# Optimization experiments

Measured on AMD Instinct MI355X. Metric: run time of the kernel, lower is better.

## Reference

```python
import jax, jax.numpy as jnp
import numpy as np

BATCH = 4096
FEAT = 1024
HID = 1024


def setup_inputs() -> dict:
    key = jax.random.key(0)
    ks = jax.random.split(key, 11)
    s_x = 1.0 / np.sqrt(FEAT)
    s_h = 1.0 / np.sqrt(HID)
    return {
        "x": jax.random.normal(ks[0], (BATCH, FEAT), jnp.float32),
        "h_prev": jax.random.normal(ks[1], (BATCH, HID), jnp.float32),
        "c_prev": jax.random.normal(ks[2], (BATCH, HID), jnp.float32),
        # Dense(3*hidden) on x and h (keras Dense: y = x @ W + b)
        "W_ifo_x": jax.random.normal(ks[3], (FEAT, 3 * HID), jnp.float32) * s_x,
        "b_ifo_x": jnp.zeros((3 * HID,), jnp.float32),
        "W_ifo_h": jax.random.normal(ks[4], (HID, 3 * HID), jnp.float32) * s_h,
        "b_ifo_h": jnp.zeros((3 * HID,), jnp.float32),
        # Dense(hidden) on x and h for candidate 'a'
        "W_b_x": jax.random.normal(ks[5], (FEAT, HID), jnp.float32) * s_x,
        "b_b_x": jnp.zeros((HID,), jnp.float32),
        "W_b_h": jax.random.normal(ks[6], (HID, HID), jnp.float32) * s_h,
        "b_b_h": jnp.zeros((HID,), jnp.float32),
    }


def reference(x, h_prev, c_prev, W_ifo_x, b_ifo_x, W_ifo_h, b_ifo_h,
              W_b_x, b_b_x, W_b_h, b_b_h):
    # Fused gate projections: [B, 3H]
    ifo = jax.nn.sigmoid(x @ W_ifo_x + b_ifo_x + h_prev @ W_ifo_h + b_ifo_h)
    i, f, o = jnp.split(ifo, 3, axis=-1)
    a = jnp.tanh(x @ W_b_x + b_b_x + h_prev @ W_b_h + b_b_h)
    c = i * a + f * c_prev
    h = o * jnp.tanh(c)
    return (h, c)
```

## Files before the change

kernel.cpp:

```cpp
#include <hip/hip_runtime.h>
#include <hip/hip_bf16.h>
#include <stdint.h>
#include <stddef.h>


#define BATCH 4096
#define FEAT  1024
#define HID   1024
#define NCAT  4096
#define KCAT  2048

typedef __attribute__((ext_vector_type(8))) __bf16 bf16x8;
typedef __attribute__((ext_vector_type(4))) float  floatx4;

__device__ __forceinline__ unsigned short f2bf(float f) {
    __hip_bfloat16 b = __float2bfloat16(f);
    return *reinterpret_cast<unsigned short*>(&b);
}
__device__ __forceinline__ void gl2lds16(const unsigned short* g, unsigned short* l) {
    __builtin_amdgcn_global_load_lds(
        (const __attribute__((address_space(1))) void*)g,
        (__attribute__((address_space(3))) void*)l, 16, 0, 0);
}

#define TP_PAD 72
__global__ __launch_bounds__(256)
void pack_all(const float* __restrict__ x, const float* __restrict__ h,
              const float* __restrict__ Wix, const float* __restrict__ Wih,
              const float* __restrict__ Wbx, const float* __restrict__ Wbh,
              unsigned short* __restrict__ Xcat, unsigned short* __restrict__ Wt) {
    __shared__ unsigned short tile[64 * TP_PAD];
    const int t = threadIdx.x;
    const int b = blockIdx.x;
    if (b < BATCH) {
        const int m = b;
        const float* src = (t < 128) ? (x + (size_t)m * FEAT + t * 8)
                                     : (h + (size_t)m * HID + (t - 128) * 8);
        float4 v0 = *(const float4*)src;
        float4 v1 = *(const float4*)(src + 4);
        union { unsigned short s16[8]; uint4 v; } pk;
        pk.s16[0] = f2bf(v0.x); pk.s16[1] = f2bf(v0.y);
        pk.s16[2] = f2bf(v0.z); pk.s16[3] = f2bf(v0.w);
        pk.s16[4] = f2bf(v1.x); pk.s16[5] = f2bf(v1.y);
        pk.s16[6] = f2bf(v1.z); pk.s16[7] = f2bf(v1.w);
        *(uint4*)(Xcat + (size_t)m * KCAT + t * 8) = pk.v;
        return;
    }
    const int tid = b - BATCH;
    const int k0  = (tid & 31) * 64;
    const int q0  = (tid >> 5) * 64;
    const float* src; int stride, cb;
    if (q0 < 3072) { src = (k0 < FEAT) ? Wix : Wih; stride = 3072; cb = q0; }
    else           { src = (k0 < FEAT) ? Wbx : Wbh; stride = 1024; cb = q0 - 3072; }
    const int krow = (k0 < FEAT) ? k0 : (k0 - FEAT);
    {
        int kl = t >> 2;
        int c0 = (t & 3) * 16;
        const float* s = src + (size_t)(krow + kl) * stride + cb + c0;
        union { unsigned short s16[16]; uint4 v[2]; } tmp;
#pragma unroll
        for (int u = 0; u < 16; u += 4) {
            float4 v = *(const float4*)(s + u);
            tmp.s16[u + 0] = f2bf(v.x); tmp.s16[u + 1] = f2bf(v.y);
            tmp.s16[u + 2] = f2bf(v.z); tmp.s16[u + 3] = f2bf(v.w);
        }
        *(uint4*)&tile[kl * TP_PAD + c0]     = tmp.v[0];
        *(uint4*)&tile[kl * TP_PAD + c0 + 8] = tmp.v[1];
    }
    __syncthreads();
    {
        int nl = t >> 2, seg = t & 3;
        int q = q0 + nl;
        int g, j;
        if (q < 3072) { g = q >> 10; j = q & 1023; }
        else          { g = 3;       j = q - 3072; }
        int np = ((j >> 4) << 6) + (g << 4) + (j & 15);
        union { unsigned short s16[16]; uint4 v[2]; } pk;
#pragma unroll
        for (int u = 0; u < 16; ++u)
            pk.s16[u] = tile[(seg * 16 + u) * TP_PAD + nl];
        uint4* dst = (uint4*)(Wt + (size_t)np * KCAT + k0 + seg * 16);
        dst[0] = pk.v[0];
        dst[1] = pk.v[1];
    }
}

#define BM 128
#define BN 128
#define BK 32

__global__ __launch_bounds__(256)
void lstm_fused(const unsigned short* __restrict__ Xcat,
                const unsigned short* __restrict__ Wt,
                const float* __restrict__ c_prev,
                const float* __restrict__ bix, const float* __restrict__ bih,
                const float* __restrict__ bbx, const float* __restrict__ bbh,
                float* __restrict__ out_h, float* __restrict__ out_c) {
    __shared__ unsigned short As[BM * BK];
    __shared__ unsigned short Bs[BN * BK];
    const int t    = threadIdx.x;
    const int lane = t & 63;
    const int wave = t >> 6;
    const int wm   = (wave >> 1) * 64;
    const int wn   = (wave & 1) * 64;
    const int m0   = blockIdx.y * BM;
    const int n0   = blockIdx.x * BN;

    floatx4 acc[4][4];
#pragma unroll
    for (int i = 0; i < 4; ++i)
#pragma unroll
        for (int g = 0; g < 4; ++g) acc[i][g] = (floatx4){0.f, 0.f, 0.f, 0.f};

    const int lrow = t >> 2;
    const int cg   = ((t & 3) ^ (lrow + (lrow >> 2))) & 3;
    const int lcol = cg * 8;

    const int lm  = lane & 15;
    const int fcs = ((lane >> 4) ^ (lm + (lm >> 2))) & 3;

    for (int kk = 0; kk < KCAT; kk += BK) {
        __syncthreads();
        gl2lds16(Xcat + (size_t)(m0 + lrow)      * KCAT + kk + lcol, &As[t * 8]);
        gl2lds16(Xcat + (size_t)(m0 + lrow + 64) * KCAT + kk + lcol, &As[t * 8 + 2048]);
        gl2lds16(Wt   + (size_t)(n0 + lrow)      * KCAT + kk + lcol, &Bs[t * 8]);
        gl2lds16(Wt   + (size_t)(n0 + lrow + 64) * KCAT + kk + lcol, &Bs[t * 8 + 2048]);
        __syncthreads();

        bf16x8 a[4], b[4];
#pragma unroll
        for (int i = 0; i < 4; ++i)
            a[i] = *(const bf16x8*)&As[(wm + i * 16 + lm) * BK + fcs * 8];
#pragma unroll
        for (int g = 0; g < 4; ++g)
            b[g] = *(const bf16x8*)&Bs[(wn + g * 16 + lm) * BK + fcs * 8];
#pragma unroll
        for (int i = 0; i < 4; ++i)
#pragma unroll
            for (int g = 0; g < 4; ++g)
                acc[i][g] = __builtin_amdgcn_mfma_f32_16x16x32_bf16(a[i], b[g], acc[i][g], 0, 0, 0);
    }

    const int j  = (((n0 + wn) >> 6) << 4) + lm;
    const float bi = bix[j]           + bih[j];
    const float bf = bix[HID + j]     + bih[HID + j];
    const float bo = bix[2 * HID + j] + bih[2 * HID + j];
    const float ba = bbx[j]           + bbh[j];
#pragma unroll
    for (int i = 0; i < 4; ++i) {
#pragma unroll
        for (int r = 0; r < 4; ++r) {
            int m = m0 + wm + i * 16 + ((lane >> 4) * 4) + r;
            float pi = acc[i][0][r] + bi;
            float pf = acc[i][1][r] + bf;
            float po = acc[i][2][r] + bo;
            float pa = acc[i][3][r] + ba;
            float ig = 1.f / (1.f + __expf(-pi));
            float fg = 1.f / (1.f + __expf(-pf));
            float og = 1.f / (1.f + __expf(-po));
            float av = 2.f / (1.f + __expf(-2.f * pa)) - 1.f;
            float cp = c_prev[(size_t)m * HID + j];
            float cv = ig * av + fg * cp;
            float hv = og * (2.f / (1.f + __expf(-2.f * cv)) - 1.f);
            out_h[(size_t)m * HID + j] = hv;
            out_c[(size_t)m * HID + j] = cv;
        }
    }
}

__global__ void naive_lstm(const float* __restrict__ x, const float* __restrict__ h,
                           const float* __restrict__ cvp,
                           const float* __restrict__ Wix, const float* __restrict__ bix,
                           const float* __restrict__ Wih, const float* __restrict__ bih,
                           const float* __restrict__ Wbx, const float* __restrict__ bbx,
                           const float* __restrict__ Wbh, const float* __restrict__ bbh,
                           float* __restrict__ out_h, float* __restrict__ out_c) {
    const int j = blockIdx.x * 256 + threadIdx.x;
    const int m = blockIdx.y;
    float ai = 0.f, af = 0.f, ao = 0.f, aa = 0.f;
    for (int k = 0; k < FEAT; ++k) {
        float xk = x[(size_t)m * FEAT + k];
        ai += xk * Wix[(size_t)k * 3072 + j];
        af += xk * Wix[(size_t)k * 3072 + HID + j];
        ao += xk * Wix[(size_t)k * 3072 + 2 * HID + j];
        aa += xk * Wbx[(size_t)k * HID + j];
    }
    for (int k = 0; k < HID; ++k) {
        float hk = h[(size_t)m * HID + k];
        ai += hk * Wih[(size_t)k * 3072 + j];
        af += hk * Wih[(size_t)k * 3072 + HID + j];
        ao += hk * Wih[(size_t)k * 3072 + 2 * HID + j];
        aa += hk * Wbh[(size_t)k * HID + j];
    }
    ai += bix[j] + bih[j];
    af += bix[HID + j] + bih[HID + j];
    ao += bix[2 * HID + j] + bih[2 * HID + j];
    aa += bbx[j] + bbh[j];
    float ig = 1.f / (1.f + __expf(-ai));
    float fg = 1.f / (1.f + __expf(-af));
    float og = 1.f / (1.f + __expf(-ao));
    float av = 2.f / (1.f + __expf(-2.f * aa)) - 1.f;
    float cp = cvp[(size_t)m * HID + j];
    float cc = ig * av + fg * cp;
    float hh = og * (2.f / (1.f + __expf(-2.f * cc)) - 1.f);
    out_h[(size_t)m * HID + j] = hh;
    out_c[(size_t)m * HID + j] = cc;
}

extern "C" void kernel_launch(void* const* d_in, const int* in_sizes, int n_in,
                              void* d_out, int out_size, void* d_ws, size_t ws_size,
                              hipStream_t stream) {
    const float* x   = (const float*)d_in[0];
    const float* h   = (const float*)d_in[1];
    const float* c   = (const float*)d_in[2];
    const float* Wix = (const float*)d_in[3];
    const float* bix = (const float*)d_in[4];
    const float* Wih = (const float*)d_in[5];
    const float* bih = (const float*)d_in[6];
    const float* Wbx = (const float*)d_in[7];
    const float* bbx = (const float*)d_in[8];
    const float* Wbh = (const float*)d_in[9];
    const float* bbh = (const float*)d_in[10];

    float* out_h = (float*)d_out;
    float* out_c = out_h + (size_t)BATCH * HID;

    const size_t WT_BYTES = (size_t)NCAT * KCAT * 2;
    const size_t XC_BYTES = (size_t)BATCH * KCAT * 2;
    if (ws_size >= WT_BYTES + XC_BYTES) {
        unsigned short* Wt   = (unsigned short*)d_ws;
        unsigned short* Xcat = (unsigned short*)((char*)d_ws + WT_BYTES);
        pack_all<<<BATCH + 2048, 256, 0, stream>>>(x, h, Wix, Wih, Wbx, Wbh, Xcat, Wt);
        lstm_fused<<<dim3(NCAT / BN, BATCH / BM), 256, 0, stream>>>(
            Xcat, Wt, c, bix, bih, bbx, bbh, out_h, out_c);
    } else {
        naive_lstm<<<dim3(HID / 256, BATCH), 256, 0, stream>>>(
            x, h, c, Wix, bix, Wih, bih, Wbx, bbx, Wbh, bbh, out_h, out_c);
    }
}
```

Before: 228.8 us.

## Fuse activation bf16 conversion into GEMM A-tile loads, drop Xcat packing

Removes the separate pass that converts x and h_prev to a concatenated bf16 buffer. The GEMM kernel now loads fp32 activations directly from global memory, converts them to bf16 in registers, and stores them to LDS, while the weights still use the async global-to-LDS path. This saves a full write and re-read of the activation buffer, but every N-tile block re-reads the fp32 activations (twice the bytes of bf16) and runs the conversion redundantly. The synchronous register loads also add latency inside the main loop, and the LDS swizzle patterns change.

Measured after the change: 292.5 us. 1.28x slower.

```diff
diff --git a/kernel.cpp b/kernel.cpp
--- a/kernel.cpp
+++ b/kernel.cpp
@@ -25,30 +25,13 @@
 
 #define TP_PAD 72
 __global__ __launch_bounds__(256)
-void pack_all(const float* __restrict__ x, const float* __restrict__ h,
-              const float* __restrict__ Wix, const float* __restrict__ Wih,
-              const float* __restrict__ Wbx, const float* __restrict__ Wbh,
-              unsigned short* __restrict__ Xcat, unsigned short* __restrict__ Wt) {
+void wt_pack(const float* __restrict__ Wix, const float* __restrict__ Wih,
+             const float* __restrict__ Wbx, const float* __restrict__ Wbh,
+             unsigned short* __restrict__ Wt) {
     __shared__ unsigned short tile[64 * TP_PAD];
-    const int t = threadIdx.x;
-    const int b = blockIdx.x;
-    if (b < BATCH) {
-        const int m = b;
-        const float* src = (t < 128) ? (x + (size_t)m * FEAT + t * 8)
-                                     : (h + (size_t)m * HID + (t - 128) * 8);
-        float4 v0 = *(const float4*)src;
-        float4 v1 = *(const float4*)(src + 4);
-        union { unsigned short s16[8]; uint4 v; } pk;
-        pk.s16[0] = f2bf(v0.x); pk.s16[1] = f2bf(v0.y);
-        pk.s16[2] = f2bf(v0.z); pk.s16[3] = f2bf(v0.w);
-        pk.s16[4] = f2bf(v1.x); pk.s16[5] = f2bf(v1.y);
-        pk.s16[6] = f2bf(v1.z); pk.s16[7] = f2bf(v1.w);
-        *(uint4*)(Xcat + (size_t)m * KCAT + t * 8) = pk.v;
-        return;
-    }
-    const int tid = b - BATCH;
-    const int k0  = (tid & 31) * 64;
-    const int q0  = (tid >> 5) * 64;
+    const int t  = threadIdx.x;
+    const int k0 = (blockIdx.x & 31) * 64;
+    const int q0 = (blockIdx.x >> 5) * 64;
     const float* src; int stride, cb;
     if (q0 < 3072) { src = (k0 < FEAT) ? Wix : Wih; stride = 3072; cb = q0; }
     else           { src = (k0 < FEAT) ? Wbx : Wbh; stride = 1024; cb = q0 - 3072; }
@@ -89,8 +72,17 @@
 #define BN 128
 #define BK 32
 
+__device__ __forceinline__ uint4 cvt8(float4 a, float4 b) {
+    union { unsigned short s16[8]; uint4 v; } pk;
+    pk.s16[0] = f2bf(a.x); pk.s16[1] = f2bf(a.y);
+    pk.s16[2] = f2bf(a.z); pk.s16[3] = f2bf(a.w);
+    pk.s16[4] = f2bf(b.x); pk.s16[5] = f2bf(b.y);
+    pk.s16[6] = f2bf(b.z); pk.s16[7] = f2bf(b.w);
+    return pk.v;
+}
+
 __global__ __launch_bounds__(256)
-void lstm_fused(const unsigned short* __restrict__ Xcat,
+void lstm_fused(const float* __restrict__ x, const float* __restrict__ hp,
                 const unsigned short* __restrict__ Wt,
                 const float* __restrict__ c_prev,
                 const float* __restrict__ bix, const float* __restrict__ bih,
@@ -112,28 +104,40 @@
 #pragma unroll
         for (int g = 0; g < 4; ++g) acc[i][g] = (floatx4){0.f, 0.f, 0.f, 0.f};
 
-    const int lrow = t >> 2;
-    const int cg   = ((t & 3) ^ (lrow + (lrow >> 2))) & 3;
-    const int lcol = cg * 8;
-
-    const int lm  = lane & 15;
-    const int fcs = ((lane >> 4) ^ (lm + (lm >> 2))) & 3;
+    const int r    = t >> 2;
+    const int p    = t & 3;
+    const int lsub = ((p ^ (r & 3)) * 8);
+    const int bcol = p * 8;
+
+    const int lm = lane & 15;
+    const int qh = lane >> 4;
+    const int pa = ((qh ^ (lm & 3)) * 8);
+    const int pb = qh * 8;
 
     for (int kk = 0; kk < KCAT; kk += BK) {
+        const float* Arow = (kk < FEAT)
+            ? (x  + (size_t)(m0 + r) * FEAT + kk + lsub)
+            : (hp + (size_t)(m0 + r) * FEAT + (kk - FEAT) + lsub);
+        float4 a0 = *(const float4*)Arow;
+        float4 a1 = *(const float4*)(Arow + 4);
+        float4 a2 = *(const float4*)(Arow + (size_t)64 * FEAT);
+        float4 a3 = *(const float4*)(Arow + (size_t)64 * FEAT + 4);
+        uint4 c0 = cvt8(a0, a1);
+        uint4 c1 = cvt8(a2, a3);
         __syncthreads();
-        gl2lds16(Xcat + (size_t)(m0 + lrow)      * KCAT + kk + lcol, &As[t * 8]);
-        gl2lds16(Xcat + (size_t)(m0 + lrow + 64) * KCAT + kk + lcol, &As[t * 8 + 2048]);
-        gl2lds16(Wt   + (size_t)(n0 + lrow)      * KCAT + kk + lcol, &Bs[t * 8]);
-        gl2lds16(Wt   + (size_t)(n0 + lrow + 64) * KCAT + kk + lcol, &Bs[t * 8 + 2048]);
+        gl2lds16(Wt + (size_t)(n0 + r)      * KCAT + kk + bcol, &Bs[t * 8]);
+        gl2lds16(Wt + (size_t)(n0 + r + 64) * KCAT + kk + bcol, &Bs[t * 8 + 2048]);
+        *(uint4*)&As[r * BK + p * 8]          = c0;
+        *(uint4*)&As[(r + 64) * BK + p * 8]   = c1;
         __syncthreads();
 
         bf16x8 a[4], b[4];
 #pragma unroll
         for (int i = 0; i < 4; ++i)
-            a[i] = *(const bf16x8*)&As[(wm + i * 16 + lm) * BK + fcs * 8];
+            a[i] = *(const bf16x8*)&As[(wm + i * 16 + lm) * BK + pa];
 #pragma unroll
         for (int g = 0; g < 4; ++g)
-            b[g] = *(const bf16x8*)&Bs[(wn + g * 16 + lm) * BK + fcs * 8];
+            b[g] = *(const bf16x8*)&Bs[(wn + g * 16 + lm) * BK + pb];
 #pragma unroll
         for (int i = 0; i < 4; ++i)
 #pragma unroll
@@ -149,16 +153,16 @@
 #pragma unroll
     for (int i = 0; i < 4; ++i) {
 #pragma unroll
-        for (int r = 0; r < 4; ++r) {
-            int m = m0 + wm + i * 16 + ((lane >> 4) * 4) + r;
-            float pi = acc[i][0][r] + bi;
-            float pf = acc[i][1][r] + bf;
-            float po = acc[i][2][r] + bo;
-            float pa = acc[i][3][r] + ba;
+        for (int rr = 0; rr < 4; ++rr) {
+            int m = m0 + wm + i * 16 + (qh * 4) + rr;
+            float pi = acc[i][0][rr] + bi;
+            float pf = acc[i][1][rr] + bf;
+            float po = acc[i][2][rr] + bo;
+            float pa2 = acc[i][3][rr] + ba;
             float ig = 1.f / (1.f + __expf(-pi));
             float fg = 1.f / (1.f + __expf(-pf));
             float og = 1.f / (1.f + __expf(-po));
-            float av = 2.f / (1.f + __expf(-2.f * pa)) - 1.f;
+            float av = 2.f / (1.f + __expf(-2.f * pa2)) - 1.f;
             float cp = c_prev[(size_t)m * HID + j];
             float cv = ig * av + fg * cp;
             float hv = og * (2.f / (1.f + __expf(-2.f * cv)) - 1.f);
@@ -226,13 +230,11 @@
     float* out_c = out_h + (size_t)BATCH * HID;
 
     const size_t WT_BYTES = (size_t)NCAT * KCAT * 2;
-    const size_t XC_BYTES = (size_t)BATCH * KCAT * 2;
-    if (ws_size >= WT_BYTES + XC_BYTES) {
-        unsigned short* Wt   = (unsigned short*)d_ws;
-        unsigned short* Xcat = (unsigned short*)((char*)d_ws + WT_BYTES);
-        pack_all<<<BATCH + 2048, 256, 0, stream>>>(x, h, Wix, Wih, Wbx, Wbh, Xcat, Wt);
+    if (ws_size >= WT_BYTES) {
+        unsigned short* Wt = (unsigned short*)d_ws;
+        wt_pack<<<2048, 256, 0, stream>>>(Wix, Wih, Wbx, Wbh, Wt);
         lstm_fused<<<dim3(NCAT / BN, BATCH / BM), 256, 0, stream>>>(
-            Xcat, Wt, c, bix, bih, bbx, bbh, out_h, out_c);
+            x, h, Wt, c, bix, bih, bbx, bbh, out_h, out_c);
     } else {
         naive_lstm<<<dim3(HID / 256, BATCH), 256, 0, stream>>>(
             x, h, c, Wix, bix, Wih, bih, Wbx, bbx, Wbh, bbh, out_h, out_c);
```

## Switch to 32x32x16 MFMA with grouped tile order and batched row packing

Applied to the files above, without the earlier changes.

The GEMM inner loop moves from 16x16x32 bf16 MFMA tiles to 32x32x16 tiles, giving four MFMAs per k-substep and fewer LDS fragment loads. The epilogue uses lane shuffles to regroup the i/f/o/a gate values. The grid becomes 1D with a grouped block-index swizzle meant to improve L2 reuse. The pack kernel now converts 8 activation rows per block, which cuts its block count. The cost is a different swizzle and output layout mapping that must still match, plus added shuffle work in the epilogue.

Result: slower. 234.4 us (+2.4%).

```diff
diff --git a/kernel.cpp b/kernel.cpp
--- a/kernel.cpp
+++ b/kernel.cpp
@@ -10,8 +10,8 @@
 #define NCAT  4096
 #define KCAT  2048
 
-typedef __attribute__((ext_vector_type(8))) __bf16 bf16x8;
-typedef __attribute__((ext_vector_type(4))) float  floatx4;
+typedef __attribute__((ext_vector_type(8)))  __bf16 bf16x8;
+typedef __attribute__((ext_vector_type(16))) float  floatx16;
 
 __device__ __forceinline__ unsigned short f2bf(float f) {
     __hip_bfloat16 b = __float2bfloat16(f);
@@ -32,23 +32,26 @@
     __shared__ unsigned short tile[64 * TP_PAD];
     const int t = threadIdx.x;
     const int b = blockIdx.x;
-    if (b < BATCH) {
-        const int m = b;
-        const float* src = (t < 128) ? (x + (size_t)m * FEAT + t * 8)
-                                     : (h + (size_t)m * HID + (t - 128) * 8);
-        float4 v0 = *(const float4*)src;
-        float4 v1 = *(const float4*)(src + 4);
-        union { unsigned short s16[8]; uint4 v; } pk;
-        pk.s16[0] = f2bf(v0.x); pk.s16[1] = f2bf(v0.y);
-        pk.s16[2] = f2bf(v0.z); pk.s16[3] = f2bf(v0.w);
-        pk.s16[4] = f2bf(v1.x); pk.s16[5] = f2bf(v1.y);
-        pk.s16[6] = f2bf(v1.z); pk.s16[7] = f2bf(v1.w);
-        *(uint4*)(Xcat + (size_t)m * KCAT + t * 8) = pk.v;
+    if (b >= 2048) {
+        const int rb = (b - 2048) * 8;
+#pragma unroll
+        for (int it = 0; it < 8; ++it) {
+            const int m = rb + it;
+            const float* src = (t < 128) ? (x + (size_t)m * FEAT + t * 8)
+                                         : (h + (size_t)m * HID + (t - 128) * 8);
+            float4 v0 = *(const float4*)src;
+            float4 v1 = *(const float4*)(src + 4);
+            union { unsigned short s16[8]; uint4 v; } pk;
+            pk.s16[0] = f2bf(v0.x); pk.s16[1] = f2bf(v0.y);
+            pk.s16[2] = f2bf(v0.z); pk.s16[3] = f2bf(v0.w);
+            pk.s16[4] = f2bf(v1.x); pk.s16[5] = f2bf(v1.y);
+            pk.s16[6] = f2bf(v1.z); pk.s16[7] = f2bf(v1.w);
+            *(uint4*)(Xcat + (size_t)m * KCAT + t * 8) = pk.v;
+        }
         return;
     }
-    const int tid = b - BATCH;
-    const int k0  = (tid & 31) * 64;
-    const int q0  = (tid >> 5) * 64;
+    const int k0 = (b & 31) * 64;
+    const int q0 = (b >> 5) * 64;
     const float* src; int stride, cb;
     if (q0 < 3072) { src = (k0 < FEAT) ? Wix : Wih; stride = 3072; cb = q0; }
     else           { src = (k0 < FEAT) ? Wbx : Wbh; stride = 1024; cb = q0 - 3072; }
@@ -103,62 +106,79 @@
     const int wave = t >> 6;
     const int wm   = (wave >> 1) * 64;
     const int wn   = (wave & 1) * 64;
-    const int m0   = blockIdx.y * BM;
-    const int n0   = blockIdx.x * BN;
-
-    floatx4 acc[4][4];
-#pragma unroll
-    for (int i = 0; i < 4; ++i)
-#pragma unroll
-        for (int g = 0; g < 4; ++g) acc[i][g] = (floatx4){0.f, 0.f, 0.f, 0.f};
-
-    const int lrow = t >> 2;
-    const int cg   = ((t & 3) ^ (lrow + (lrow >> 2))) & 3;
-    const int lcol = cg * 8;
-
-    const int lm  = lane & 15;
-    const int fcs = ((lane >> 4) ^ (lm + (lm >> 2))) & 3;
+
+    const int id = blockIdx.x;
+    const int grp = id >> 4;
+    const int bm = (grp & 7) * 4 + ((id >> 2) & 3);
+    const int bn = (grp >> 3) * 4 + (id & 3);
+    const int m0 = bm * BM;
+    const int n0 = bn * BN;
+
+    floatx16 acc[2][2];
+#pragma unroll
+    for (int i = 0; i < 2; ++i)
+#pragma unroll
+        for (int n = 0; n < 2; ++n)
+#pragma unroll
+            for (int q = 0; q < 16; ++q) acc[i][n][q] = 0.f;
+
+    const int r  = t >> 2;
+    const int cA = (((t & 3) ^ ((r >> 1) & 3)) * 8);
+
+    const int rl  = lane & 31;
+    const int hi  = lane >> 5;
+    const int swz = (rl >> 1) & 3;
 
     for (int kk = 0; kk < KCAT; kk += BK) {
         __syncthreads();
-        gl2lds16(Xcat + (size_t)(m0 + lrow)      * KCAT + kk + lcol, &As[t * 8]);
-        gl2lds16(Xcat + (size_t)(m0 + lrow + 64) * KCAT + kk + lcol, &As[t * 8 + 2048]);
-        gl2lds16(Wt   + (size_t)(n0 + lrow)      * KCAT + kk + lcol, &Bs[t * 8]);
-        gl2lds16(Wt   + (size_t)(n0 + lrow + 64) * KCAT + kk + lcol, &Bs[t * 8 + 2048]);
+        gl2lds16(Xcat + (size_t)(m0 + r)      * KCAT + kk + cA, &As[t * 8]);
+        gl2lds16(Xcat + (size_t)(m0 + r + 64) * KCAT + kk + cA, &As[t * 8 + 2048]);
+        gl2lds16(Wt   + (size_t)(n0 + r)      * KCAT + kk + cA, &Bs[t * 8]);
+        gl2lds16(Wt   + (size_t)(n0 + r + 64) * KCAT + kk + cA, &Bs[t * 8 + 2048]);
         __syncthreads();
 
-        bf16x8 a[4], b[4];
-#pragma unroll
-        for (int i = 0; i < 4; ++i)
-            a[i] = *(const bf16x8*)&As[(wm + i * 16 + lm) * BK + fcs * 8];
-#pragma unroll
-        for (int g = 0; g < 4; ++g)
-            b[g] = *(const bf16x8*)&Bs[(wn + g * 16 + lm) * BK + fcs * 8];
-#pragma unroll
-        for (int i = 0; i < 4; ++i)
-#pragma unroll
-            for (int g = 0; g < 4; ++g)
-                acc[i][g] = __builtin_amdgcn_mfma_f32_16x16x32_bf16(a[i], b[g], acc[i][g], 0, 0, 0);
-    }
-
-    const int j  = (((n0 + wn) >> 6) << 4) + lm;
+#pragma unroll
+        for (int ks = 0; ks < 2; ++ks) {
+            const int co = (((ks * 2 + hi) ^ swz) * 8);
+            bf16x8 a0 = *(const bf16x8*)&As[(wm +      rl) * BK + co];
+            bf16x8 a1 = *(const bf16x8*)&As[(wm + 32 + rl) * BK + co];
+            bf16x8 b0 = *(const bf16x8*)&Bs[(wn +      rl) * BK + co];
+            bf16x8 b1 = *(const bf16x8*)&Bs[(wn + 32 + rl) * BK + co];
+            acc[0][0] = __builtin_amdgcn_mfma_f32_32x32x16_bf16(a0, b0, acc[0][0], 0, 0, 0);
+            acc[0][1] = __builtin_amdgcn_mfma_f32_32x32x16_bf16(a0, b1, acc[0][1], 0, 0, 0);
+            acc[1][0] = __builtin_amdgcn_mfma_f32_32x32x16_bf16(a1, b0, acc[1][0], 0, 0, 0);
+            acc[1][1] = __builtin_amdgcn_mfma_f32_32x32x16_bf16(a1, b1, acc[1][1], 0, 0, 0);
+        }
+    }
+
+    const int hl = (lane >> 4) & 1;
+    const int jc = lane & 15;
+    const int j  = (((n0 + wn) >> 6) << 4) + jc;
     const float bi = bix[j]           + bih[j];
     const float bf = bix[HID + j]     + bih[HID + j];
     const float bo = bix[2 * HID + j] + bih[2 * HID + j];
     const float ba = bbx[j]           + bbh[j];
-#pragma unroll
-    for (int i = 0; i < 4; ++i) {
-#pragma unroll
-        for (int r = 0; r < 4; ++r) {
-            int m = m0 + wm + i * 16 + ((lane >> 4) * 4) + r;
-            float pi = acc[i][0][r] + bi;
-            float pf = acc[i][1][r] + bf;
-            float po = acc[i][2][r] + bo;
-            float pa = acc[i][3][r] + ba;
-            float ig = 1.f / (1.f + __expf(-pi));
-            float fg = 1.f / (1.f + __expf(-pf));
-            float og = 1.f / (1.f + __expf(-po));
-            float av = 2.f / (1.f + __expf(-2.f * pa)) - 1.f;
+    const int mbase = m0 + wm + hl * 32 + 4 * hi;
+#pragma unroll
+    for (int q = 0; q < 4; ++q) {
+#pragma unroll
+        for (int rr = 0; rr < 4; ++rr) {
+            const int reg = q * 4 + rr;
+            const int m   = mbase + q * 8 + rr;
+            float own0  = hl ? acc[1][0][reg] : acc[0][0][reg];
+            float own1  = hl ? acc[1][1][reg] : acc[0][1][reg];
+            float send0 = hl ? acc[0][0][reg] : acc[1][0][reg];
+            float send1 = hl ? acc[0][1][reg] : acc[1][1][reg];
+            float recv0 = __shfl_xor(send0, 16, 64);
+            float recv1 = __shfl_xor(send1, 16, 64);
+            float gi = (hl ? recv0 : own0) + bi;
+            float gf = (hl ? own0 : recv0) + bf;
+            float go = (hl ? recv1 : own1) + bo;
+            float ga = (hl ? own1 : recv1) + ba;
+            float ig = 1.f / (1.f + __expf(-gi));
+            float fg = 1.f / (1.f + __expf(-gf));
+            float og = 1.f / (1.f + __expf(-go));
+            float av = 2.f / (1.f + __expf(-2.f * ga)) - 1.f;
             float cp = c_prev[(size_t)m * HID + j];
             float cv = ig * av + fg * cp;
             float hv = og * (2.f / (1.f + __expf(-2.f * cv)) - 1.f);
@@ -230,8 +250,8 @@
     if (ws_size >= WT_BYTES + XC_BYTES) {
         unsigned short* Wt   = (unsigned short*)d_ws;
         unsigned short* Xcat = (unsigned short*)((char*)d_ws + WT_BYTES);
-        pack_all<<<BATCH + 2048, 256, 0, stream>>>(x, h, Wix, Wih, Wbx, Wbh, Xcat, Wt);
-        lstm_fused<<<dim3(NCAT / BN, BATCH / BM), 256, 0, stream>>>(
+        pack_all<<<2048 + 512, 256, 0, stream>>>(x, h, Wix, Wih, Wbx, Wbh, Xcat, Wt);
+        lstm_fused<<<1024, 256, 0, stream>>>(
             Xcat, Wt, c, bix, bih, bbx, bbh, out_h, out_c);
     } else {
         naive_lstm<<<dim3(HID / 256, BATCH), 256, 0, stream>>>(
```
